# Optimization experiments

Hardware: AMD Instinct MI355X
Metric: run time of the kernel (lower is better)

Reference implementation:

```python
import jax, jax.numpy as jnp
import numpy as np

EPS = 1e-5

def _rmsnorm(x):
    # BitLinear applies a (non-learnable) RMSNorm to activations before quantization
    return x * jax.lax.rsqrt(jnp.mean(x * x, axis=-1, keepdims=True) + EPS)

def _activation_quant(x):
    # per-token absmax int8 quantization, dequantized back to float
    scale = 127.0 / jnp.clip(jnp.max(jnp.abs(x), axis=-1, keepdims=True), EPS, None)
    return jnp.clip(jnp.round(x * scale), -128, 127) / scale

def _weight_quant(w):
    # absmean ternary {-1,0,1} quantization, dequantized back to float
    scale = 1.0 / jnp.clip(jnp.mean(jnp.abs(w)), EPS, None)
    return jnp.clip(jnp.round(w * scale), -1, 1) / scale

def _bitlinear(x, w):
    xn = _rmsnorm(x)
    # straight-through estimators (identity grads through quantizers)
    xq = xn + jax.lax.stop_gradient(_activation_quant(xn) - xn)
    wq = w + jax.lax.stop_gradient(_weight_quant(w) - w)
    return jnp.einsum('bsd,hd->bsh', xq, wq)

def setup_inputs() -> dict:
    key = jax.random.key(0)
    k1, k2, k3, k4 = jax.random.split(key, 4)
    B, S, D, H = 4, 2048, 4096, 11008
    return {
        'x': jax.random.normal(k1, (B, S, D), dtype=jnp.float32),
        'w_gate': jax.random.normal(k2, (H, D), dtype=jnp.float32) * 0.02,
        'w_up': jax.random.normal(k3, (H, D), dtype=jnp.float32) * 0.02,
        'w_down': jax.random.normal(k4, (D, H), dtype=jnp.float32) * 0.02,
    }

def reference(x, w_gate, w_up, w_down):
    h = jax.nn.silu(_bitlinear(x, w_gate)) * _bitlinear(x, w_up)
    return _bitlinear(h, w_down)
```

## Files before the change

### kernel.cpp

```cpp
#include <hip/hip_runtime.h>
#include <hip/hip_bf16.h>
#include <cstdint>

#define EPS 1e-5

typedef __attribute__((ext_vector_type(4))) int int32x4;

__device__ __forceinline__ void gload(const char* g, char* l) {
  __builtin_amdgcn_global_load_lds(
      (const __attribute__((address_space(1))) unsigned int*)g,
      (__attribute__((address_space(3))) unsigned int*)l, 16, 0, 0);
}

__device__ inline float np_leaf_abs(const float* __restrict__ a, int n) {
  float r[8];
  #pragma unroll
  for (int j = 0; j < 8; j++) r[j] = fabsf(a[j]);
  for (int i = 8; i < n; i += 8) {
    #pragma unroll
    for (int j = 0; j < 8; j++) r[j] += fabsf(a[i + j]);
  }
  return ((r[0] + r[1]) + (r[2] + r[3])) + ((r[4] + r[5]) + (r[6] + r[7]));
}

__global__ __launch_bounds__(256) void np_blocksums3(
    const float* __restrict__ w0, const float* __restrict__ w1,
    const float* __restrict__ w2, float* __restrict__ bs) {
  int b = blockIdx.x * 256 + threadIdx.x;
  const float* w = (b < 131072) ? w0 : (b < 262144 ? w1 : w2);
  long lb = b & 131071;
  const float* a = w + lb * 344;
  float s0 = np_leaf_abs(a, 80);
  float s1 = np_leaf_abs(a + 80, 88);
  float s2 = np_leaf_abs(a + 168, 88);
  float s3 = np_leaf_abs(a + 256, 88);
  bs[b] = (s0 + s1) + (s2 + s3);
}

__global__ __launch_bounds__(256) void np_tree_partial3(
    const float* __restrict__ bs, float* __restrict__ part) {
  __shared__ float sh[256];
  int t = threadIdx.x;
  const float* a = bs + (long)blockIdx.x * 512;
  sh[t] = a[2 * t] + a[2 * t + 1];
  __syncthreads();
  for (int n = 128; n >= 1; n >>= 1) {
    float x = 0.f;
    if (t < n) x = sh[2 * t] + sh[2 * t + 1];
    __syncthreads();
    if (t < n) sh[t] = x;
    __syncthreads();
  }
  if (t == 0) part[blockIdx.x] = sh[0];
}

__global__ __launch_bounds__(128) void np_tree_final3(
    const float* __restrict__ part, float* __restrict__ meanw) {
  __shared__ float sh[128];
  int t = threadIdx.x;
  const float* p = part + blockIdx.x * 256;
  sh[t] = p[2 * t] + p[2 * t + 1];
  __syncthreads();
  for (int n = 64; n >= 1; n >>= 1) {
    float x = 0.f;
    if (t < n) x = sh[2 * t] + sh[2 * t + 1];
    __syncthreads();
    if (t < n) sh[t] = x;
    __syncthreads();
  }
  if (t == 0) meanw[blockIdx.x] = sh[0] / 45088768.0f;
}

__global__ __launch_bounds__(256) void quant_w_gu(
    const float* __restrict__ wg, const float* __restrict__ wu,
    const float* __restrict__ meanw, char* __restrict__ qg, char* __restrict__ qu,
    long n4) {
  int half = (blockIdx.x >= 4096);
  const float* w = half ? wu : wg;
  char* q = half ? qu : qg;
  float scale = 1.0f / fmaxf(meanw[half], 1e-5f);
  long i = (long)(blockIdx.x & 4095) * blockDim.x + threadIdx.x;
  long stride = 4096L * blockDim.x;
  const float4* w4 = (const float4*)w;
  char4* q4 = (char4*)q;
  for (; i < n4; i += stride) {
    float4 v = w4[i];
    char4 c;
    c.x = (char)(int)fminf(1.f, fmaxf(-1.f, rintf(v.x * scale)));
    c.y = (char)(int)fminf(1.f, fmaxf(-1.f, rintf(v.y * scale)));
    c.z = (char)(int)fminf(1.f, fmaxf(-1.f, rintf(v.z * scale)));
    c.w = (char)(int)fminf(1.f, fmaxf(-1.f, rintf(v.w * scale)));
    q4[i] = c;
  }
}

#define CORR_MAX 1024
#define WIN 1e-6f

__global__ __launch_bounds__(256) void quant_w_down(
    const float* __restrict__ w, const float* __restrict__ mean_ptr,
    char* __restrict__ q, int* __restrict__ cnt,
    int* __restrict__ ck, float* __restrict__ cv) {
  float scale = 1.0f / fmaxf(mean_ptr[2], 1e-5f);
  long i0 = ((long)blockIdx.x * blockDim.x + threadIdx.x) * 4;
  long stride = (long)gridDim.x * blockDim.x * 4;
  for (long i = i0; i < 4096L * 11008L; i += stride) {
    char4 c;
    #pragma unroll
    for (int j = 0; j < 4; j++) {
      float t = w[i + j] * scale;
      float qv = fminf(1.f, fmaxf(-1.f, rintf(t)));
      if (fabsf(fabsf(t) - 0.5f) < WIN) {
        qv = 0.f;
        int idx = atomicAdd(cnt, 1);
        if (idx < CORR_MAX) {
          ck[idx] = (int)(i + j);
          cv[idx] = t > 0.f ? 0.5f : -0.5f;
        }
      }
      ((char*)&c)[j] = (char)(int)qv;
    }
    *(char4*)(q + i) = c;
  }
}

__global__ void zero_cnt(int* cnt) { *cnt = 0; }

__global__ __launch_bounds__(64) void apply_corr(
    const int* __restrict__ cnt, const int* __restrict__ ck,
    const float* __restrict__ cv, const char* __restrict__ qh,
    const float* __restrict__ fh, const float* __restrict__ meanw,
    float* __restrict__ out) {
  int r = blockIdx.x * 64 + threadIdx.x;
  float fwd = fmaxf(meanw[2], 1e-5f);
  int n = *cnt; if (n > CORR_MAX) n = CORR_MAX;
  float fr = fh[r] * fwd;
  for (int i = 0; i < n; i++) {
    int flat = ck[i];
    int nn = flat / 11008, kk = flat % 11008;
    float qv = (float)qh[(long)r * 11008 + kk];
    out[(long)r * 4096 + nn] += cv[i] * qv * fr;
  }
}

__device__ inline void block_reduce_sum_max_d(double& s, float& m) {
  #pragma unroll
  for (int off = 1; off < 64; off <<= 1) {
    s += __shfl_xor(s, off, 64);
    m = fmaxf(m, __shfl_xor(m, off, 64));
  }
  __shared__ double ssh[4];
  __shared__ float msh[4];
  int wv = threadIdx.x >> 6;
  if ((threadIdx.x & 63) == 0) { ssh[wv] = s; msh[wv] = m; }
  __syncthreads();
  s = (ssh[0] + ssh[1]) + (ssh[2] + ssh[3]);
  m = fmaxf(fmaxf(msh[0], msh[1]), fmaxf(msh[2], msh[3]));
}

__device__ inline char quant1d(float x, double rn, double s) {
  double t = (double)x * rn;
  double q = rint(t * s);
  q = fmin(127.0, fmax(-128.0, q));
  return (char)(int)q;
}

__global__ __launch_bounds__(256) void act_quant_x(
    const float* __restrict__ x, char* __restrict__ qx, float* __restrict__ fx) {
  const int row = blockIdx.x;
  const float4* xr = (const float4*)(x + (long)row * 4096);
  float4 v[4];
  double ss = 0.0;
  float am = 0.f;
  #pragma unroll
  for (int i = 0; i < 4; i++) {
    v[i] = xr[i * 256 + threadIdx.x];
    ss += ((double)v[i].x * v[i].x + (double)v[i].y * v[i].y) +
          ((double)v[i].z * v[i].z + (double)v[i].w * v[i].w);
    am = fmaxf(am, fmaxf(fmaxf(fabsf(v[i].x), fabsf(v[i].y)),
                         fmaxf(fabsf(v[i].z), fabsf(v[i].w))));
  }
  block_reduce_sum_max_d(ss, am);
  double rn = 1.0 / sqrt(ss / 4096.0 + EPS);
  double den = fmax((double)am * rn, EPS);
  double s = 127.0 / den;
  if (threadIdx.x == 0) fx[row] = (float)(den / 127.0);
  char4* qr = (char4*)(qx + (long)row * 4096);
  #pragma unroll
  for (int i = 0; i < 4; i++) {
    char4 c;
    c.x = quant1d(v[i].x, rn, s);
    c.y = quant1d(v[i].y, rn, s);
    c.z = quant1d(v[i].z, rn, s);
    c.w = quant1d(v[i].w, rn, s);
    qr[i * 256 + threadIdx.x] = c;
  }
}

__global__ __launch_bounds__(256) void act_quant_h(
    const float* __restrict__ h, char* __restrict__ qh, float* __restrict__ fh) {
  __shared__ float4 hrow4[2752];
  const long row = blockIdx.x;
  const float4* hr = (const float4*)(h + row * 11008);
  double ss = 0.0;
  float am = 0.f;
  for (int i = threadIdx.x; i < 2752; i += 256) {
    float4 v = hr[i];
    hrow4[i] = v;
    ss += ((double)v.x * v.x + (double)v.y * v.y) +
          ((double)v.z * v.z + (double)v.w * v.w);
    am = fmaxf(am, fmaxf(fmaxf(fabsf(v.x), fabsf(v.y)),
                         fmaxf(fabsf(v.z), fabsf(v.w))));
  }
  block_reduce_sum_max_d(ss, am);
  double rn = 1.0 / sqrt(ss / 11008.0 + EPS);
  double den = fmax((double)am * rn, EPS);
  double s = 127.0 / den;
  if (threadIdx.x == 0) fh[row] = (float)(den / 127.0);
  char4* qr = (char4*)(qh + row * 11008);
  for (int i = threadIdx.x; i < 2752; i += 256) {
    float4 v = hrow4[i];
    char4 c;
    c.x = quant1d(v.x, rn, s);
    c.y = quant1d(v.y, rn, s);
    c.z = quant1d(v.z, rn, s);
    c.w = quant1d(v.w, rn, s);
    qr[i] = c;
  }
}


__global__ __launch_bounds__(256, 2) void gemm_gateup(
    const char* __restrict__ qx, const char* __restrict__ qwg, const char* __restrict__ qwu,
    const float* __restrict__ meanw, const float* __restrict__ fx, float* __restrict__ h) {
  __shared__ __align__(16) char As[3][8192];
  __shared__ __align__(16) char Bgs[3][8192];
  __shared__ __align__(16) char Bus[3][8192];
  const int t = threadIdx.x;
  const int lane = t & 63;
  const int wv = t >> 6;
  const int bid = blockIdx.x;
  const int swz = (bid & 7) * 688 + (bid >> 3);
  const int m0 = (swz & 63) * 128;
  const int n0 = (swz >> 6) * 128;
  const int wm = (wv >> 1) * 64;
  const int wn = (wv & 1) * 64;

  const int rowin = lane >> 2;
  const int gcol = (((lane & 3) - ((lane >> 3) & 3)) & 3) * 16;
  const int loff = (lane & 15) * 64 + ((((lane >> 4) + ((lane >> 1) & 3)) & 3) << 4);

  const char* gA = qx  + (long)(m0 + wv * 32 + rowin) * 4096 + gcol;
  const char* gG = qwg + (long)(n0 + wv * 32 + rowin) * 4096 + gcol;
  const char* gU = qwu + (long)(n0 + wv * 32 + rowin) * 4096 + gcol;
  const long R16 = 16L * 4096;

  int32x4 accg[4][4] = {};
  int32x4 accu[4][4] = {};
  int32x4 a0[4], g0[4], u0[4], a1[4], g1[4], u1[4];

  char *PA0 = &As[0][0], *PA1 = &As[1][0], *PA2 = &As[2][0];
  char *PG0 = &Bgs[0][0], *PG1 = &Bgs[1][0], *PG2 = &Bgs[2][0];
  char *PU0 = &Bus[0][0], *PU1 = &Bus[1][0], *PU2 = &Bus[2][0];

  #define GU_STAGE(pa, pg, pu, k0)                          \
    do {                                                    \
      gload(gA + (k0),       (pa) + wv * 2048);             \
      gload(gA + (k0) + R16, (pa) + wv * 2048 + 1024);      \
      gload(gG + (k0),       (pg) + wv * 2048);             \
      gload(gG + (k0) + R16, (pg) + wv * 2048 + 1024);      \
      gload(gU + (k0),       (pu) + wv * 2048);             \
      gload(gU + (k0) + R16, (pu) + wv * 2048 + 1024);      \
    } while (0)

  #define GU_READ(ar, gr, ur, pa, pg, pu)                          \
    do {                                                           \
      _Pragma("unroll")                                            \
      for (int m = 0; m < 4; m++)                                  \
        ar[m] = *(const int32x4*)((pa) + (wm + m * 16) * 64 + loff); \
      _Pragma("unroll")                                            \
      for (int n = 0; n < 4; n++) {                                \
        gr[n] = *(const int32x4*)((pg) + (wn + n * 16) * 64 + loff); \
        ur[n] = *(const int32x4*)((pu) + (wn + n * 16) * 64 + loff); \
      }                                                            \
    } while (0)

  #define GU_MFMA(ar, gr, ur)                                                \
    do {                                                                     \
      __builtin_amdgcn_s_setprio(1);                                         \
      _Pragma("unroll")                                                      \
      for (int n = 0; n < 4; n++) {                                          \
        _Pragma("unroll")                                                    \
        for (int m = 0; m < 4; m++) {                                        \
          accg[m][n] = __builtin_amdgcn_mfma_i32_16x16x64_i8(ar[m], gr[n], accg[m][n], 0, 0, 0); \
          accu[m][n] = __builtin_amdgcn_mfma_i32_16x16x64_i8(ar[m], ur[n], accu[m][n], 0, 0, 0); \
        }                                                                    \
      }                                                                      \
      __builtin_amdgcn_s_setprio(0);                                         \
    } while (0)

  #define GU_ROT()                                          \
    do {                                                    \
      char* tp;                                             \
      tp = PA0; PA0 = PA1; PA1 = PA2; PA2 = tp;             \
      tp = PG0; PG0 = PG1; PG1 = PG2; PG2 = tp;             \
      tp = PU0; PU0 = PU1; PU1 = PU2; PU2 = tp;             \
    } while (0)

  #define GU_BODY(ks, Rc_a, Rc_g, Rc_u, Rn_a, Rn_g, Rn_u)          \
    do {                                                           \
      if ((ks) + 3 < 64) GU_STAGE(PA0, PG0, PU0, ((ks) + 3) * 64); \
      if ((ks) + 1 < 64) GU_READ(Rn_a, Rn_g, Rn_u, PA1, PG1, PU1); \
      GU_MFMA(Rc_a, Rc_g, Rc_u);                                   \
      if ((ks) + 3 < 64) asm volatile("s_waitcnt vmcnt(6)" ::: "memory"); \
      else               asm volatile("s_waitcnt vmcnt(0)" ::: "memory"); \
      if ((ks) < 62) __builtin_amdgcn_s_barrier();                 \
      GU_ROT();                                                    \
    } while (0)

  GU_STAGE(PA0, PG0, PU0, 0);
  GU_STAGE(PA1, PG1, PU1, 64);
  GU_STAGE(PA2, PG2, PU2, 128);
  asm volatile("s_waitcnt vmcnt(12)" ::: "memory");
  __builtin_amdgcn_s_barrier();
  GU_READ(a0, g0, u0, PA0, PG0, PU0);
  asm volatile("s_waitcnt vmcnt(6)" ::: "memory");
  __builtin_amdgcn_s_barrier();

  for (int ks = 0; ks < 64; ks += 2) {
    GU_BODY(ks,     a0, g0, u0, a1, g1, u1);
    GU_BODY(ks + 1, a1, g1, u1, a0, g0, u0);
  }
  #undef GU_STAGE
  #undef GU_READ
  #undef GU_MFMA
  #undef GU_ROT
  #undef GU_BODY

  float fwg = fmaxf(meanw[0], 1e-5f);
  float fwu = fmaxf(meanw[1], 1e-5f);
  const int rgrp = lane >> 4;
  const int cidx = lane & 15;
  #pragma unroll
  for (int m = 0; m < 4; m++) {
    #pragma unroll
    for (int r = 0; r < 4; r++) {
      int grow = m0 + wm + m * 16 + rgrp * 4 + r;
      float fxr = fx[grow];
      float sg = fxr * fwg, su = fxr * fwu;
      #pragma unroll
      for (int n = 0; n < 4; n++) {
        float g = (float)accg[m][n][r] * sg;
        float u = (float)accu[m][n][r] * su;
        float hv = g / (1.f + expf(-g)) * u;
        h[(long)grow * 11008 + (n0 + wn + n * 16 + cidx)] = hv;
      }
    }
  }
}

__global__ __launch_bounds__(256, 2) void gemm_down(
    const char* __restrict__ qh, const char* __restrict__ qwd,
    const float* __restrict__ meanw, const float* __restrict__ fh,
    float* __restrict__ out) {
  __shared__ __align__(16) char As[3][8192];
  __shared__ __align__(16) char Bs[3][16384];
  const int t = threadIdx.x;
  const int lane = t & 63;
  const int wv = t >> 6;
  const int bid = blockIdx.x;
  const int swz = (bid & 7) * 128 + (bid >> 3);
  const int m0 = (swz & 63) * 128;
  const int n0 = (swz >> 6) * 256;
  const int wm = (wv >> 1) * 64;
  const int wn = (wv & 1) * 128;

  const int rowin = lane >> 2;
  const int gcol = (((lane & 3) - ((lane >> 3) & 3)) & 3) * 16;
  const int loff = (lane & 15) * 64 + ((((lane >> 4) + ((lane >> 1) & 3)) & 3) << 4);

  const char* gA = qh  + (long)(m0 + wv * 32 + rowin) * 11008 + gcol;
  const char* gB = qwd + (long)(n0 + wv * 64 + rowin) * 11008 + gcol;
  const long R16 = 16L * 11008;

  int32x4 acc[4][8] = {};
  int32x4 a0[4], b0[8], a1[4], b1[8];

  char *PA0 = &As[0][0], *PA1 = &As[1][0], *PA2 = &As[2][0];
  char *PB0 = &Bs[0][0], *PB1 = &Bs[1][0], *PB2 = &Bs[2][0];

  #define DN_STAGE(pa, pb, k0)                              \
    do {                                                    \
      gload(gA + (k0),           (pa) + wv * 2048);         \
      gload(gA + (k0) + R16,     (pa) + wv * 2048 + 1024);  \
      gload(gB + (k0),           (pb) + wv * 4096);         \
      gload(gB + (k0) + R16,     (pb) + wv * 4096 + 1024);  \
      gload(gB + (k0) + 2 * R16, (pb) + wv * 4096 + 2048);  \
      gload(gB + (k0) + 3 * R16, (pb) + wv * 4096 + 3072);  \
    } while (0)

  #define DN_READ(ar, br, pa, pb)                                   \
    do {                                                            \
      _Pragma("unroll")                                             \
      for (int m = 0; m < 4; m++)                                   \
        ar[m] = *(const int32x4*)((pa) + (wm + m * 16) * 64 + loff);\
      _Pragma("unroll")                                             \
      for (int n = 0; n < 8; n++)                                   \
        br[n] = *(const int32x4*)((pb) + (wn + n * 16) * 64 + loff);\
    } while (0)

  #define DN_MFMA(ar, br)                                                    \
    do {                                                                     \
      __builtin_amdgcn_s_setprio(1);                                         \
      _Pragma("unroll")                                                      \
      for (int n = 0; n < 8; n++) {                                          \
        _Pragma("unroll")                                                    \
        for (int m = 0; m < 4; m++)                                          \
          acc[m][n] = __builtin_amdgcn_mfma_i32_16x16x64_i8(ar[m], br[n], acc[m][n], 0, 0, 0); \
      }                                                                      \
      __builtin_amdgcn_s_setprio(0);                                         \
    } while (0)

  #define DN_ROT()                                          \
    do {                                                    \
      char* tp;                                             \
      tp = PA0; PA0 = PA1; PA1 = PA2; PA2 = tp;             \
      tp = PB0; PB0 = PB1; PB1 = PB2; PB2 = tp;             \
    } while (0)

  #define DN_BODY(ks, Rc_a, Rc_b, Rn_a, Rn_b)                      \
    do {                                                           \
      if ((ks) + 3 < 172) DN_STAGE(PA0, PB0, ((ks) + 3) * 64);     \
      if ((ks) + 1 < 172) DN_READ(Rn_a, Rn_b, PA1, PB1);           \
      DN_MFMA(Rc_a, Rc_b);                                         \
      if ((ks) + 3 < 172) asm volatile("s_waitcnt vmcnt(6)" ::: "memory"); \
      else                asm volatile("s_waitcnt vmcnt(0)" ::: "memory"); \
      if ((ks) < 170) __builtin_amdgcn_s_barrier();                \
      DN_ROT();                                                    \
    } while (0)

  DN_STAGE(PA0, PB0, 0);
  DN_STAGE(PA1, PB1, 64);
  DN_STAGE(PA2, PB2, 128);
  asm volatile("s_waitcnt vmcnt(12)" ::: "memory");
  __builtin_amdgcn_s_barrier();
  DN_READ(a0, b0, PA0, PB0);
  asm volatile("s_waitcnt vmcnt(6)" ::: "memory");
  __builtin_amdgcn_s_barrier();

  for (int ks = 0; ks < 172; ks += 2) {
    DN_BODY(ks,     a0, b0, a1, b1);
    DN_BODY(ks + 1, a1, b1, a0, b0);
  }
  #undef DN_STAGE
  #undef DN_READ
  #undef DN_MFMA
  #undef DN_ROT
  #undef DN_BODY

  float fwd = fmaxf(meanw[2], 1e-5f);
  const int rgrp = lane >> 4;
  const int cidx = lane & 15;
  #pragma unroll
  for (int m = 0; m < 4; m++) {
    #pragma unroll
    for (int r = 0; r < 4; r++) {
      int grow = m0 + wm + m * 16 + rgrp * 4 + r;
      float f = fh[grow] * fwd;
      #pragma unroll
      for (int n = 0; n < 8; n++) {
        out[(long)grow * 4096 + (n0 + wn + n * 16 + cidx)] =
            (float)acc[m][n][r] * f;
      }
    }
  }
}

extern "C" void kernel_launch(void* const* d_in, const int* in_sizes, int n_in,
                              void* d_out, int out_size, void* d_ws, size_t ws_size,
                              hipStream_t stream) {
  const float* x      = (const float*)d_in[0];
  const float* w_gate = (const float*)d_in[1];
  const float* w_up   = (const float*)d_in[2];
  const float* w_down = (const float*)d_in[3];
  float* out = (float*)d_out;

  const long NW = 11008L * 4096L;
  const long NX = 8192L * 4096L;
  const long NH = 8192L * 11008L;

  char* ws  = (char*)d_ws;
  char* qwg = ws;
  char* qwu = qwg + NW;
  char* qwd = qwu + NW;
  char* qx  = qwd + NW;
  char* qh  = qx + NX;
  float* h  = (float*)(qh + NH);
  float* fx = h + NH;
  float* fh = fx + 8192;
  float* meanw = fh + 8192;
  float* bs    = meanw + 4;
  float* part  = bs + 3 * 131072;
  int*   ccnt  = (int*)(part + 1024);
  int*   ck    = ccnt + 4;
  float* cv    = (float*)(ck + CORR_MAX);

  zero_cnt<<<1, 1, 0, stream>>>(ccnt);

  np_blocksums3<<<1536, 256, 0, stream>>>(w_gate, w_up, w_down, bs);
  np_tree_partial3<<<768, 256, 0, stream>>>(bs, part);
  np_tree_final3<<<3, 128, 0, stream>>>(part, meanw);

  quant_w_gu<<<8192, 256, 0, stream>>>(w_gate, w_up, meanw, qwg, qwu, NW / 4);
  quant_w_down<<<4096, 256, 0, stream>>>(w_down, meanw, qwd, ccnt, ck, cv);

  act_quant_x<<<8192, 256, 0, stream>>>(x, qx, fx);

  gemm_gateup<<<5504, 256, 0, stream>>>(qx, qwg, qwu, meanw, fx, h);

  act_quant_h<<<8192, 256, 0, stream>>>(h, qh, fh);

  gemm_down<<<1024, 256, 0, stream>>>(qh, qwd, meanw, fh, out);

  apply_corr<<<128, 64, 0, stream>>>(ccnt, ck, cv, qh, fh, meanw, out);
}
```

Before: 1.690 ms.

## Replace LDS-staged triple-buffered GEMM pipeline with direct global-to-register loads

Removes the shared-memory staging (global_load_lds into triple-buffered LDS, with waitcnt and barriers) from both int8 GEMM kernels. Each wave now loads its MFMA operand fragments straight from global memory into registers, double-buffered across k-steps. This drops the LDS traffic and the barriers, but the wave pairs that share rows no longer share loaded tiles. Every wave fetches its own A and B fragments, which raises global/L2 traffic and exposes load latency to the MFMA loop.

```diff
diff --git a/kernel.cpp b/kernel.cpp
--- a/kernel.cpp
+++ b/kernel.cpp
@@ -5,12 +5,6 @@
 #define EPS 1e-5
 
 typedef __attribute__((ext_vector_type(4))) int int32x4;
-
-__device__ __forceinline__ void gload(const char* g, char* l) {
-  __builtin_amdgcn_global_load_lds(
-      (const __attribute__((address_space(1))) unsigned int*)g,
-      (__attribute__((address_space(3))) unsigned int*)l, 16, 0, 0);
-}
 
 __device__ inline float np_leaf_abs(const float* __restrict__ a, int n) {
   float r[8];
@@ -233,9 +227,6 @@
 __global__ __launch_bounds__(256, 2) void gemm_gateup(
     const char* __restrict__ qx, const char* __restrict__ qwg, const char* __restrict__ qwu,
     const float* __restrict__ meanw, const float* __restrict__ fx, float* __restrict__ h) {
-  __shared__ __align__(16) char As[3][8192];
-  __shared__ __align__(16) char Bgs[3][8192];
-  __shared__ __align__(16) char Bus[3][8192];
   const int t = threadIdx.x;
   const int lane = t & 63;
   const int wv = t >> 6;
@@ -246,43 +237,28 @@
   const int wm = (wv >> 1) * 64;
   const int wn = (wv & 1) * 64;
 
-  const int rowin = lane >> 2;
-  const int gcol = (((lane & 3) - ((lane >> 3) & 3)) & 3) * 16;
-  const int loff = (lane & 15) * 64 + ((((lane >> 4) + ((lane >> 1) & 3)) & 3) << 4);
-
-  const char* gA = qx  + (long)(m0 + wv * 32 + rowin) * 4096 + gcol;
-  const char* gG = qwg + (long)(n0 + wv * 32 + rowin) * 4096 + gcol;
-  const char* gU = qwu + (long)(n0 + wv * 32 + rowin) * 4096 + gcol;
-  const long R16 = 16L * 4096;
+  const int r15 = lane & 15;
+  const int kb = (lane >> 4) * 16;
+
+  const char* pA = qx  + (long)(m0 + wm + r15) * 4096 + kb;
+  const char* pG = qwg + (long)(n0 + wn + r15) * 4096 + kb;
+  const char* pU = qwu + (long)(n0 + wn + r15) * 4096 + kb;
+  const long RS = 16L * 4096;
 
   int32x4 accg[4][4] = {};
   int32x4 accu[4][4] = {};
   int32x4 a0[4], g0[4], u0[4], a1[4], g1[4], u1[4];
 
-  char *PA0 = &As[0][0], *PA1 = &As[1][0], *PA2 = &As[2][0];
-  char *PG0 = &Bgs[0][0], *PG1 = &Bgs[1][0], *PG2 = &Bgs[2][0];
-  char *PU0 = &Bus[0][0], *PU1 = &Bus[1][0], *PU2 = &Bus[2][0];
-
-  #define GU_STAGE(pa, pg, pu, k0)                          \
-    do {                                                    \
-      gload(gA + (k0),       (pa) + wv * 2048);             \
-      gload(gA + (k0) + R16, (pa) + wv * 2048 + 1024);      \
-      gload(gG + (k0),       (pg) + wv * 2048);             \
-      gload(gG + (k0) + R16, (pg) + wv * 2048 + 1024);      \
-      gload(gU + (k0),       (pu) + wv * 2048);             \
-      gload(gU + (k0) + R16, (pu) + wv * 2048 + 1024);      \
-    } while (0)
-
-  #define GU_READ(ar, gr, ur, pa, pg, pu)                          \
-    do {                                                           \
-      _Pragma("unroll")                                            \
-      for (int m = 0; m < 4; m++)                                  \
-        ar[m] = *(const int32x4*)((pa) + (wm + m * 16) * 64 + loff); \
-      _Pragma("unroll")                                            \
-      for (int n = 0; n < 4; n++) {                                \
-        gr[n] = *(const int32x4*)((pg) + (wn + n * 16) * 64 + loff); \
-        ur[n] = *(const int32x4*)((pu) + (wn + n * 16) * 64 + loff); \
-      }                                                            \
+  #define GU_LOAD(ar, gr, ur, k0)                              \
+    do {                                                       \
+      _Pragma("unroll")                                        \
+      for (int m = 0; m < 4; m++)                              \
+        ar[m] = *(const int32x4*)(pA + m * RS + (k0));         \
+      _Pragma("unroll")                                        \
+      for (int n = 0; n < 4; n++) {                            \
+        gr[n] = *(const int32x4*)(pG + n * RS + (k0));         \
+        ur[n] = *(const int32x4*)(pU + n * RS + (k0));         \
+      }                                                        \
     } while (0)
 
   #define GU_MFMA(ar, gr, ur)                                                \
@@ -299,43 +275,15 @@
       __builtin_amdgcn_s_setprio(0);                                         \
     } while (0)
 
-  #define GU_ROT()                                          \
-    do {                                                    \
-      char* tp;                                             \
-      tp = PA0; PA0 = PA1; PA1 = PA2; PA2 = tp;             \
-      tp = PG0; PG0 = PG1; PG1 = PG2; PG2 = tp;             \
-      tp = PU0; PU0 = PU1; PU1 = PU2; PU2 = tp;             \
-    } while (0)
-
-  #define GU_BODY(ks, Rc_a, Rc_g, Rc_u, Rn_a, Rn_g, Rn_u)          \
-    do {                                                           \
-      if ((ks) + 3 < 64) GU_STAGE(PA0, PG0, PU0, ((ks) + 3) * 64); \
-      if ((ks) + 1 < 64) GU_READ(Rn_a, Rn_g, Rn_u, PA1, PG1, PU1); \
-      GU_MFMA(Rc_a, Rc_g, Rc_u);                                   \
-      if ((ks) + 3 < 64) asm volatile("s_waitcnt vmcnt(6)" ::: "memory"); \
-      else               asm volatile("s_waitcnt vmcnt(0)" ::: "memory"); \
-      if ((ks) < 62) __builtin_amdgcn_s_barrier();                 \
-      GU_ROT();                                                    \
-    } while (0)
-
-  GU_STAGE(PA0, PG0, PU0, 0);
-  GU_STAGE(PA1, PG1, PU1, 64);
-  GU_STAGE(PA2, PG2, PU2, 128);
-  asm volatile("s_waitcnt vmcnt(12)" ::: "memory");
-  __builtin_amdgcn_s_barrier();
-  GU_READ(a0, g0, u0, PA0, PG0, PU0);
-  asm volatile("s_waitcnt vmcnt(6)" ::: "memory");
-  __builtin_amdgcn_s_barrier();
-
+  GU_LOAD(a0, g0, u0, 0);
   for (int ks = 0; ks < 64; ks += 2) {
-    GU_BODY(ks,     a0, g0, u0, a1, g1, u1);
-    GU_BODY(ks + 1, a1, g1, u1, a0, g0, u0);
-  }
-  #undef GU_STAGE
-  #undef GU_READ
+    if (ks + 1 < 64) GU_LOAD(a1, g1, u1, (ks + 1) * 64);
+    GU_MFMA(a0, g0, u0);
+    if (ks + 2 < 64) GU_LOAD(a0, g0, u0, (ks + 2) * 64);
+    GU_MFMA(a1, g1, u1);
+  }
+  #undef GU_LOAD
   #undef GU_MFMA
-  #undef GU_ROT
-  #undef GU_BODY
 
   float fwg = fmaxf(meanw[0], 1e-5f);
   float fwu = fmaxf(meanw[1], 1e-5f);
@@ -363,8 +311,6 @@
     const char* __restrict__ qh, const char* __restrict__ qwd,
     const float* __restrict__ meanw, const float* __restrict__ fh,
     float* __restrict__ out) {
-  __shared__ __align__(16) char As[3][8192];
-  __shared__ __align__(16) char Bs[3][16384];
   const int t = threadIdx.x;
   const int lane = t & 63;
   const int wv = t >> 6;
@@ -375,38 +321,24 @@
   const int wm = (wv >> 1) * 64;
   const int wn = (wv & 1) * 128;
 
-  const int rowin = lane >> 2;
-  const int gcol = (((lane & 3) - ((lane >> 3) & 3)) & 3) * 16;
-  const int loff = (lane & 15) * 64 + ((((lane >> 4) + ((lane >> 1) & 3)) & 3) << 4);
-
-  const char* gA = qh  + (long)(m0 + wv * 32 + rowin) * 11008 + gcol;
-  const char* gB = qwd + (long)(n0 + wv * 64 + rowin) * 11008 + gcol;
-  const long R16 = 16L * 11008;
+  const int r15 = lane & 15;
+  const int kb = (lane >> 4) * 16;
+
+  const char* pA = qh  + (long)(m0 + wm + r15) * 11008 + kb;
+  const char* pB = qwd + (long)(n0 + wn + r15) * 11008 + kb;
+  const long RS = 16L * 11008;
 
   int32x4 acc[4][8] = {};
   int32x4 a0[4], b0[8], a1[4], b1[8];
 
-  char *PA0 = &As[0][0], *PA1 = &As[1][0], *PA2 = &As[2][0];
-  char *PB0 = &Bs[0][0], *PB1 = &Bs[1][0], *PB2 = &Bs[2][0];
-
-  #define DN_STAGE(pa, pb, k0)                              \
-    do {                                                    \
-      gload(gA + (k0),           (pa) + wv * 2048);         \
-      gload(gA + (k0) + R16,     (pa) + wv * 2048 + 1024);  \
-      gload(gB + (k0),           (pb) + wv * 4096);         \
-      gload(gB + (k0) + R16,     (pb) + wv * 4096 + 1024);  \
-      gload(gB + (k0) + 2 * R16, (pb) + wv * 4096 + 2048);  \
-      gload(gB + (k0) + 3 * R16, (pb) + wv * 4096 + 3072);  \
-    } while (0)
-
-  #define DN_READ(ar, br, pa, pb)                                   \
-    do {                                                            \
-      _Pragma("unroll")                                             \
-      for (int m = 0; m < 4; m++)                                   \
-        ar[m] = *(const int32x4*)((pa) + (wm + m * 16) * 64 + loff);\
-      _Pragma("unroll")                                             \
-      for (int n = 0; n < 8; n++)                                   \
-        br[n] = *(const int32x4*)((pb) + (wn + n * 16) * 64 + loff);\
+  #define DN_LOAD(ar, br, k0)                                  \
+    do {                                                       \
+      _Pragma("unroll")                                        \
+      for (int m = 0; m < 4; m++)                              \
+        ar[m] = *(const int32x4*)(pA + m * RS + (k0));         \
+      _Pragma("unroll")                                        \
+      for (int n = 0; n < 8; n++)                              \
+        br[n] = *(const int32x4*)(pB + n * RS + (k0));         \
     } while (0)
 
   #define DN_MFMA(ar, br)                                                    \
@@ -421,42 +353,15 @@
       __builtin_amdgcn_s_setprio(0);                                         \
     } while (0)
 
-  #define DN_ROT()                                          \
-    do {                                                    \
-      char* tp;                                             \
-      tp = PA0; PA0 = PA1; PA1 = PA2; PA2 = tp;             \
-      tp = PB0; PB0 = PB1; PB1 = PB2; PB2 = tp;             \
-    } while (0)
-
-  #define DN_BODY(ks, Rc_a, Rc_b, Rn_a, Rn_b)                      \
-    do {                                                           \
-      if ((ks) + 3 < 172) DN_STAGE(PA0, PB0, ((ks) + 3) * 64);     \
-      if ((ks) + 1 < 172) DN_READ(Rn_a, Rn_b, PA1, PB1);           \
-      DN_MFMA(Rc_a, Rc_b);                                         \
-      if ((ks) + 3 < 172) asm volatile("s_waitcnt vmcnt(6)" ::: "memory"); \
-      else                asm volatile("s_waitcnt vmcnt(0)" ::: "memory"); \
-      if ((ks) < 170) __builtin_amdgcn_s_barrier();                \
-      DN_ROT();                                                    \
-    } while (0)
-
-  DN_STAGE(PA0, PB0, 0);
-  DN_STAGE(PA1, PB1, 64);
-  DN_STAGE(PA2, PB2, 128);
-  asm volatile("s_waitcnt vmcnt(12)" ::: "memory");
-  __builtin_amdgcn_s_barrier();
-  DN_READ(a0, b0, PA0, PB0);
-  asm volatile("s_waitcnt vmcnt(6)" ::: "memory");
-  __builtin_amdgcn_s_barrier();
-
+  DN_LOAD(a0, b0, 0);
   for (int ks = 0; ks < 172; ks += 2) {
-    DN_BODY(ks,     a0, b0, a1, b1);
-    DN_BODY(ks + 1, a1, b1, a0, b0);
-  }
-  #undef DN_STAGE
-  #undef DN_READ
+    if (ks + 1 < 172) DN_LOAD(a1, b1, (ks + 1) * 64);
+    DN_MFMA(a0, b0);
+    if (ks + 2 < 172) DN_LOAD(a0, b0, (ks + 2) * 64);
+    DN_MFMA(a1, b1);
+  }
+  #undef DN_LOAD
   #undef DN_MFMA
-  #undef DN_ROT
-  #undef DN_BODY
 
   float fwd = fmaxf(meanw[2], 1e-5f);
   const int rgrp = lane >> 4;
```

After: 3.315 ms. 96.2% more time.
